# Optimization experiments

Measured on AMD Instinct MI355X. Metric: run time of the kernel, lower is better.

Reference implementation:

```python
import jax, jax.numpy as jnp
import numpy as np

B, L, D = 2, 2048, 2048
HQ, HKV = 32, 8
HD = D // HQ  # 64
ROPE_BASE = 10000.0
ROPE_SCALE = 1.0


def setup_inputs() -> dict:
    key = jax.random.key(0)
    ks = jax.random.split(key, 5)
    s = 0.02
    return {
        "x": jax.random.normal(ks[0], (B, L, D), dtype=jnp.float32),
        "pos_ids": jnp.arange(L, dtype=jnp.int64) if jax.config.jax_enable_x64 else jnp.arange(L, dtype=jnp.int32),
        "wq": jax.random.normal(ks[1], (D, D), dtype=jnp.float32) * s,
        "wk": jax.random.normal(ks[2], (HKV * HD, D), dtype=jnp.float32) * s,
        "wv": jax.random.normal(ks[3], (HKV * HD, D), dtype=jnp.float32) * s,
        "wo": jax.random.normal(ks[4], (D, D), dtype=jnp.float32) * s,
    }


def _rope_cos_sin(pos_ids, rot_dim, dtype):
    half = rot_dim // 2
    idx = jnp.arange(half, dtype=jnp.float32)
    inv_freq = (1.0 / (ROPE_BASE ** (idx / half))) * ROPE_SCALE  # [half]
    freqs = pos_ids.astype(dtype)[:, None] * inv_freq.astype(dtype)[None, :]  # [L, half]
    return jnp.cos(freqs), jnp.sin(freqs)


def _apply_rotary(x, cos, sin):
    # x: [B, L, H, Hd]; interleaved pair rotation on full head dim
    b, l, h, hd = x.shape
    xp = x.reshape(b, l, h, hd // 2, 2)
    x1, x2 = xp[..., 0], xp[..., 1]
    c = cos.reshape(1, l, 1, hd // 2)
    s = sin.reshape(1, l, 1, hd // 2)
    y1 = x1 * c - x2 * s
    y2 = x1 * s + x2 * c
    return jnp.stack([y1, y2], axis=-1).reshape(b, l, h, hd)


def reference(x, pos_ids, wq, wk, wv, wo):
    b, l, d = x.shape
    q = (x @ wq.T).reshape(b, l, HQ, HD)
    k = (x @ wk.T).reshape(b, l, HKV, HD)
    v = (x @ wv.T).reshape(b, l, HKV, HD)

    cos, sin = _rope_cos_sin(pos_ids, HD, x.dtype)
    q = _apply_rotary(q, cos, sin)
    k = _apply_rotary(k, cos, sin)

    group = HQ // HKV  # GQA: each kv head serves `group` consecutive q heads
    k = jnp.repeat(k, group, axis=2)  # [b, l, HQ, HD]
    v = jnp.repeat(v, group, axis=2)

    scale = 1.0 / jnp.sqrt(jnp.asarray(HD, dtype=x.dtype))
    scores = jnp.einsum("bqhd,bkhd->bhqk", q, k) * scale  # [b, HQ, l, l]
    causal = jnp.tril(jnp.ones((l, l), dtype=bool))
    neg = jnp.asarray(jnp.finfo(x.dtype).min, dtype=x.dtype)
    scores = jnp.where(causal[None, None], scores, neg)
    attn = jax.nn.softmax(scores, axis=-1)
    out = jnp.einsum("bhqk,bkhd->bqhd", attn, v).reshape(b, l, d)
    return out @ wo.T
```

## Files before the change

### kernel.cpp

```cpp
#include <hip/hip_runtime.h>
#include <stdint.h>

typedef unsigned short u16;
typedef unsigned int   u32;
typedef __bf16 bf16_t;
typedef bf16_t bf16x8 __attribute__((ext_vector_type(8)));
typedef u16    u16x8  __attribute__((ext_vector_type(8)));
typedef float  f32x4  __attribute__((ext_vector_type(4)));
typedef float  f32x16 __attribute__((ext_vector_type(16)));

#define NB   2
#define NL   2048
#define ND   2048
#define NHQ  32
#define NHKV 8
#define NHD  64
#define NQKV 3072
#define QSCALE 0.18033688011112042f
#define SM_SHIFT 24.0f

__device__ __forceinline__ u16 f2bf(float x){
  union{float f;u32 u;} v; v.f = x;
  u32 r = v.u + 0x7FFFu + ((v.u >> 16) & 1u);
  return (u16)(r >> 16);
}
__device__ __forceinline__ float bf2f(u16 b){
  union{u32 u;float f;} v; v.u = ((u32)b) << 16; return v.f;
}

__device__ __forceinline__ float exp2_hw(float x){
#if __has_builtin(__builtin_amdgcn_exp2f)
  return __builtin_amdgcn_exp2f(x);
#else
  float r; asm("v_exp_f32 %0, %1" : "=v"(r) : "v"(x)); return r;
#endif
}

__device__ __forceinline__ void gload_lds16(const void* g, void* l){
  auto gp = reinterpret_cast<__attribute__((address_space(1))) u16*>(
      (uintptr_t)g);
  auto lp = reinterpret_cast<__attribute__((address_space(3))) u16*>(
      (uintptr_t)l);
  __builtin_amdgcn_global_load_lds(gp, lp, 16, 0, 0);
}

__device__ __forceinline__ f32x4 mfma16(bf16x8 a, bf16x8 b, f32x4 c){
  return __builtin_amdgcn_mfma_f32_16x16x32_bf16(a, b, c, 0, 0, 0);
}
__device__ __forceinline__ f32x16 mfma32(bf16x8 a, bf16x8 b, f32x16 c){
  return __builtin_amdgcn_mfma_f32_32x32x16_bf16(a, b, c, 0, 0, 0);
}
__device__ __forceinline__ u32 cvtpk(float lo, float hi){
  u32 w;
  asm("v_cvt_pk_bf16_f32 %0, %1, %2" : "=v"(w) : "v"(lo), "v"(hi));
  return w;
}

template<int N> __device__ __forceinline__ void lgkm_wait(){
  if      constexpr (N == 0)  asm volatile("s_waitcnt lgkmcnt(0)"  ::: "memory");
  else if constexpr (N == 4)  asm volatile("s_waitcnt lgkmcnt(4)"  ::: "memory");
  else if constexpr (N == 8)  asm volatile("s_waitcnt lgkmcnt(8)"  ::: "memory");
  else if constexpr (N == 12) asm volatile("s_waitcnt lgkmcnt(12)" ::: "memory");
  else if constexpr (N == 14) asm volatile("s_waitcnt lgkmcnt(14)" ::: "memory");
  else                        asm volatile("s_waitcnt lgkmcnt(15)" ::: "memory");
  __builtin_amdgcn_sched_barrier(0);
}

#define CV_S1 2097152
#define CV_S2 3145728
#define CV_S3 3407872
#define CV_S4 3670016
#define CV_S5 4718592
#define CV_TOT (CV_S5 + 65536)

__global__ void k_prep(const float* __restrict__ x,  const float* __restrict__ wq,
                       const float* __restrict__ wk, const float* __restrict__ wv,
                       const float* __restrict__ wo, const int* __restrict__ pos,
                       u16* __restrict__ xb, u16* __restrict__ wqkvb, u16* __restrict__ wob,
                       float2* __restrict__ csT){
  int i = blockIdx.x * 256 + threadIdx.x;
  if (i < CV_S5){
    const float4* src; ushort4* dst; int off;
    if (i < CV_S1)      { src = (const float4*)x;  dst = (ushort4*)xb;    off = i; }
    else if (i < CV_S2) { src = (const float4*)wq; dst = (ushort4*)wqkvb; off = i - CV_S1; }
    else if (i < CV_S3) { src = (const float4*)wk; dst = (ushort4*)wqkvb + 1048576; off = i - CV_S2; }
    else if (i < CV_S4) { src = (const float4*)wv; dst = (ushort4*)wqkvb + 1310720; off = i - CV_S3; }
    else                { src = (const float4*)wo; dst = (ushort4*)wob;   off = i - CV_S4; }
    float4 f = src[off];
    ushort4 o;
    o.x = f2bf(f.x); o.y = f2bf(f.y); o.z = f2bf(f.z); o.w = f2bf(f.w);
    dst[off] = o;
  } else {
    int idx = i - CV_S5;
    int l = idx >> 5, k = idx & 31;
    float p = (float)pos[l];
    float inv = __expf(-((float)k * (1.0f/32.0f)) * 9.210340371976184f);
    float fr = p * inv;
    csT[idx] = make_float2(cosf(fr), sinf(fr));
  }
}

template<int BM, int BN, int MODE>
__global__ __launch_bounds__(512) void k_gemm9(const u16* __restrict__ A,
                                               const u16* __restrict__ Bm,
                                               void* __restrict__ Cp,
                                               u16* __restrict__ Qo, u16* __restrict__ Ko,
                                               u16* __restrict__ VT,
                                               const float2* __restrict__ csT,
                                               int M, int N, int K){
  constexpr int LA_N = BM/64;
  constexpr int LB_N = BN/64;
  constexpr int LN   = LA_N + LB_N;
  constexpr int MR   = BM/32;
  constexpr int MH   = MR/2;
  constexpr int NF   = BN/64;
  __shared__ u16 LAb[2][BM*64];
  __shared__ u16 LBb[2][BN*64];
  const int tid = threadIdx.x;
  const int lane = tid & 63, w = tid >> 6;
  const int wr = w >> 2, wc = w & 3;
  const int lr = lane & 15, lg = lane >> 4;
  const int tn = blockIdx.x * BN, tm = blockIdx.y * BM;
  const size_t Kb = (size_t)K * 2;
  const char* Ab = (const char*)A;
  const char* Bb = (const char*)Bm;

  u32 soff[LN]; int ldoff[LN];
#pragma unroll
  for (int l = 0; l < LN; ++l){
    int o = ((l < LA_N) ? l : (l - LA_N))*8192 + tid*16;
    int s = o ^ (((o>>7)&7)<<4);
    int row = s >> 7, col = s & 127;
    int trow = (l < LA_N) ? (tm + row) : (tn + row);
    soff[l]  = (u32)((size_t)trow * Kb + col);
    ldoff[l] = o;
  }
  const int c0 = ( lg      ^ (lr & 7)) << 4;
  const int c1 = ((4 + lg) ^ (lr & 7)) << 4;
  const int arow = (wr*(BM/2) + lr) * 128;
  const int brow = (wc*(BN/4) + lr) * 128;

  f32x4 acc[MR][NF] = {};
  bf16x8 bfA[NF][2], bfB[NF][2], afA[MH][2], afB[MH][2];
  const int NT = K >> 6;

#pragma unroll
  for (int l = 0; l < LN; ++l){
    char* base = (l < LA_N) ? (char*)LAb[0] : (char*)LBb[0];
    const char* gb = (l < LA_N) ? Ab : Bb;
    gload_lds16(gb + soff[l], base + ldoff[l]);
  }
  asm volatile("s_waitcnt vmcnt(0)" ::: "memory");
  __builtin_amdgcn_s_barrier();
#pragma unroll
  for (int n = 0; n < NF; ++n){
    bfA[n][0] = *(const bf16x8*)((const char*)LBb[0] + brow + n*2048 + c0);
    bfA[n][1] = *(const bf16x8*)((const char*)LBb[0] + brow + n*2048 + c1);
  }
#pragma unroll
  for (int q = 0; q < MH; ++q){
    afA[q][0] = *(const bf16x8*)((const char*)LAb[0] + arow + q*2048 + c0);
    afA[q][1] = *(const bf16x8*)((const char*)LAb[0] + arow + q*2048 + c1);
  }

#define TILE(laC, laN, lbN, bfc, bfn, PRE, KOFF)                            \
    {                                                                       \
      if (PRE){                                                             \
        _Pragma("unroll")                                                   \
        for (int l = 0; l < LN; ++l){                                       \
          char* nb_ = (l < LA_N) ? (char*)(laN) : (char*)(lbN);             \
          const char* gb_ = (l < LA_N) ? Ab : Bb;                           \
          gload_lds16(gb_ + soff[l] + (KOFF), nb_ + ldoff[l]);              \
        }                                                                   \
      }                                                                     \
      _Pragma("unroll")                                                     \
      for (int q = 0; q < MH; ++q){                                         \
        afB[q][0] = *(const bf16x8*)((const char*)(laC) + arow + (MH+q)*2048 + c0); \
        afB[q][1] = *(const bf16x8*)((const char*)(laC) + arow + (MH+q)*2048 + c1); \
      }                                                                     \
      lgkm_wait<2*MH>();                                                    \
      __builtin_amdgcn_s_setprio(1);                                        \
      _Pragma("unroll")                                                     \
      for (int q = 0; q < MH; ++q){                                         \
        _Pragma("unroll")                                                   \
        for (int n = 0; n < NF; ++n){                                       \
          acc[q][n] = mfma16(afA[q][0], bfc[n][0], acc[q][n]);              \
          acc[q][n] = mfma16(afA[q][1], bfc[n][1], acc[q][n]);              \
        }                                                                   \
      }                                                                     \
      __builtin_amdgcn_s_setprio(0);                                        \
      asm volatile("s_waitcnt vmcnt(0)" ::: "memory");                      \
      __builtin_amdgcn_s_barrier();                                         \
      if (PRE){                                                             \
        _Pragma("unroll")                                                   \
        for (int n = 0; n < NF; ++n){                                       \
          bfn[n][0] = *(const bf16x8*)((const char*)(lbN) + brow + n*2048 + c0); \
          bfn[n][1] = *(const bf16x8*)((const char*)(lbN) + brow + n*2048 + c1); \
        }                                                                   \
        _Pragma("unroll")                                                   \
        for (int q = 0; q < MH; ++q){                                       \
          afA[q][0] = *(const bf16x8*)((const char*)(laN) + arow + q*2048 + c0); \
          afA[q][1] = *(const bf16x8*)((const char*)(laN) + arow + q*2048 + c1); \
        }                                                                   \
        lgkm_wait<2*NF + 2*MH>();                                           \
      } else {                                                              \
        lgkm_wait<0>();                                                     \
      }                                                                     \
      __builtin_amdgcn_s_setprio(1);                                        \
      _Pragma("unroll")                                                     \
      for (int q = 0; q < MH; ++q){                                         \
        _Pragma("unroll")                                                   \
        for (int n = 0; n < NF; ++n){                                       \
          acc[MH+q][n] = mfma16(afB[q][0], bfc[n][0], acc[MH+q][n]);        \
          acc[MH+q][n] = mfma16(afB[q][1], bfc[n][1], acc[MH+q][n]);        \
        }                                                                   \
      }                                                                     \
      __builtin_amdgcn_s_setprio(0);                                        \
      __builtin_amdgcn_s_barrier();                                         \
    }

#pragma unroll 1
  for (int kt = 0; kt < NT; kt += 2){
    const bool pre1 = (kt + 2 < NT);
    TILE(LAb[0], LAb[1], LBb[1], bfA, bfB, true, (u32)(kt+1)*128)
    TILE(LAb[1], LAb[0], LBb[0], bfB, bfA, pre1, (u32)(kt+2)*128)
  }
#undef TILE

  const int rb = tm + wr*(BM/2) + lg*4;
  const int cb = tn + wc*(BN/4) + lr;
#pragma unroll
  for (int m = 0; m < MR; ++m){
#pragma unroll
    for (int n = 0; n < NF; ++n){
      const int col = cb + n*16;
      if (MODE == 2){
        const int row0 = rb + m*16;
        const int bb = row0 >> 11;
        if (col >= 2560){
          const int vcol = col - 2560, kvh = vcol >> 6, d = vcol & 63;
          const int l0 = row0 & 2047;
          ushort4 sv;
          sv.x = f2bf(acc[m][n][0]); sv.y = f2bf(acc[m][n][1]);
          sv.z = f2bf(acc[m][n][2]); sv.w = f2bf(acc[m][n][3]);
          *reinterpret_cast<ushort4*>(&VT[((size_t)(bb*NHKV + kvh)*NHD + d)*NL + l0]) = sv;
        } else {
          const bool isQ = col < 2048;
          const int hcol = isQ ? col : (col - 2048);
          const int hh = hcol >> 6, d = hcol & 63;
          const int i = (d >> 1);
          const bool odd = (d & 1);
          u16* dst = isQ ? &Qo[((size_t)(bb*NHQ + hh)*NL) * NHD]
                         : &Ko[((size_t)(bb*NHKV + hh)*NL) * NHD];
#pragma unroll
          for (int r = 0; r < 4; ++r){
            const int l = (row0 + r) & 2047;
            const float2 cs = csT[l*32 + i];
            const float a = acc[m][n][r];
            const float p = __shfl_xor(a, 1);
            float y = odd ? (p*cs.y + a*cs.x) : (a*cs.x - p*cs.y);
            if (isQ) y *= QSCALE;
            dst[(size_t)l*NHD + d] = f2bf(y);
          }
        }
      } else {
#pragma unroll
        for (int r = 0; r < 4; ++r){
          size_t off = (size_t)(rb + m*16 + r) * N + col;
          ((float*)Cp)[off] = acc[m][n][r];
        }
      }
    }
  }
}

__device__ __forceinline__ void stage_kv32(const u16* __restrict__ Kp, const u16* __restrict__ VTp,
                                           int kvb, u16* lk, u16* lv, int w, int lane){
  const char* ks = (const char*)(Kp + (size_t)kvb*NHD);
  const char* vs = (const char*)VTp + (size_t)kvb*2;
  const int o = w*1024 + lane*16;
  const int swk = o ^ (((o>>7)&7)<<4);
  gload_lds16(ks + swk, (char*)lk + w*1024);
  const int row = o >> 6, c = o & 63;
  gload_lds16(vs + (size_t)row*(NL*2) + (c ^ (((row>>1)&3)<<4)), (char*)lv + w*1024);
}
__device__ __forceinline__ bf16x8 ldsK(const u16* base, int row, int colb){
  return *reinterpret_cast<const bf16x8*>((const char*)base + row*128 + (colb ^ ((row&7)<<4)));
}
__device__ __forceinline__ bf16x8 ldsV(const u16* base, int row, int colb){
  return *reinterpret_cast<const bf16x8*>((const char*)base + row*64 + (colb ^ (((row>>1)&3)<<4)));
}

__global__ __launch_bounds__(256) void k_attn7(const u16* __restrict__ Q, const u16* __restrict__ Kg,
                                               const u16* __restrict__ VT, u16* __restrict__ O){
  __shared__ u16 LK[2][2048];
  __shared__ u16 LV[2][2048];
  const int tid = threadIdx.x, lane = tid & 63, w = tid >> 6;
  const int q32 = lane & 31, hi = lane >> 5;
  const int f = blockIdx.x;
  const int round = f >> 8, c = f & 255;
  const int i16 = c >> 4;
  const int qti = round*16 + ((round & 1) ? (15 - i16) : i16);
  const int qt = 63 - qti;
  const int grp = c & 15;
  const int b = grp >> 3, kvh = grp & 7;
  const int h = kvh*4 + w;
  const u16* Qp  = Q  + ((size_t)(b*NHQ  + h  ))*NL*NHD;
  const u16* Kp  = Kg + ((size_t)(b*NHKV + kvh))*NL*NHD;
  const u16* VTp = VT + ((size_t)(b*NHKV + kvh))*NHD*NL;

  const int qrow = qt*32 + q32;
  const int ntw  = qt + 1;

  bf16x8 qf[4];
#pragma unroll
  for (int ks = 0; ks < 4; ++ks)
    qf[ks] = *reinterpret_cast<const bf16x8*>(&Qp[(size_t)qrow*NHD + ks*16 + hi*8]);

  f32x16 o0 = {}, o1 = {};
  float lsum = 0.0f;

  stage_kv32(Kp, VTp, 0, LK[0], LV[0], w, lane);
  __syncthreads();

#pragma unroll 1
  for (int j = 0; j < ntw; ++j){
    const int cur = j & 1;
    const u16* lk = LK[cur];
    const u16* lv = LV[cur];
    if (j + 1 < ntw)
      stage_kv32(Kp, VTp, (j+1) << 5, LK[cur^1], LV[cur^1], w, lane);

    const int kvb = j << 5;
    bf16x8 kf[4];
#pragma unroll
    for (int ks = 0; ks < 4; ++ks)
      kf[ks] = ldsK(lk, q32, ks*32 + hi*16);
    f32x16 s0 = {};
    __builtin_amdgcn_s_setprio(1);
#pragma unroll
    for (int ks = 0; ks < 4; ++ks)
      s0 = mfma32(kf[ks], qf[ks], s0);
    __builtin_amdgcn_s_setprio(0);
    if (j == ntw - 1){
#pragma unroll
      for (int r = 0; r < 16; ++r){
        const int kl = (r&3) + 8*(r>>2) + 4*hi;
        if (kvb + kl > qrow) s0[r] = -1e30f;
      }
    }
#pragma unroll
    for (int r = 0; r < 16; ++r) s0[r] = exp2_hw(s0[r] - SM_SHIFT);
    float u[8];
#pragma unroll
    for (int r = 0; r < 8; ++r)  u[r] = s0[r] + s0[r+8];
#pragma unroll
    for (int r = 0; r < 4; ++r)  u[r] += u[r+4];
    lsum += (u[0]+u[1]) + (u[2]+u[3]);
    u32 wds[8];
#pragma unroll
    for (int i = 0; i < 8; ++i) wds[i] = cvtpk(s0[2*i], s0[2*i+1]);
    bf16x8 pf[2];
#pragma unroll
    for (int fi = 0; fi < 2; ++fi){
      u32 x  = wds[4*fi+0], y  = wds[4*fi+2];
      u32 x2 = wds[4*fi+1], y2 = wds[4*fi+3];
      asm("v_permlane32_swap_b32 %0, %1" : "+v"(x),  "+v"(y));
      asm("v_permlane32_swap_b32 %0, %1" : "+v"(x2), "+v"(y2));
      union { u32 wq[4]; bf16x8 v; } uu;
      uu.wq[0] = x; uu.wq[1] = x2; uu.wq[2] = y; uu.wq[3] = y2;
      pf[fi] = uu.v;
    }
    bf16x8 vf[4];
    vf[0] = ldsV(lv, q32,      hi*16);
    vf[1] = ldsV(lv, q32,      32 + hi*16);
    vf[2] = ldsV(lv, 32 + q32, hi*16);
    vf[3] = ldsV(lv, 32 + q32, 32 + hi*16);
    __builtin_amdgcn_s_setprio(1);
    o0 = mfma32(vf[0], pf[0], o0);
    o0 = mfma32(vf[1], pf[1], o0);
    o1 = mfma32(vf[2], pf[0], o1);
    o1 = mfma32(vf[3], pf[1], o1);
    __builtin_amdgcn_s_setprio(0);
    __syncthreads();
  }

  float lt = lsum + __shfl_xor(lsum, 32);
  const float inv = 1.0f / lt;
  u16* Op = O + ((size_t)(b*NL + qrow))*ND + h*NHD;
#pragma unroll
  for (int md = 0; md < 2; ++md){
#pragma unroll
    for (int q4 = 0; q4 < 4; ++q4){
      ushort4 sv;
      float a0 = (md ? o1[4*q4+0] : o0[4*q4+0]) * inv;
      float a1 = (md ? o1[4*q4+1] : o0[4*q4+1]) * inv;
      float a2 = (md ? o1[4*q4+2] : o0[4*q4+2]) * inv;
      float a3 = (md ? o1[4*q4+3] : o0[4*q4+3]) * inv;
      sv.x = f2bf(a0); sv.y = f2bf(a1); sv.z = f2bf(a2); sv.w = f2bf(a3);
      *reinterpret_cast<ushort4*>(&Op[md*32 + 8*q4 + 4*hi]) = sv;
    }
  }
}

extern "C" void kernel_launch(void* const* d_in, const int* in_sizes, int n_in,
                              void* d_out, int out_size, void* d_ws, size_t ws_size,
                              hipStream_t stream){
  (void)in_sizes; (void)n_in; (void)out_size; (void)ws_size;
  const float* x   = (const float*)d_in[0];
  const int*   pos = (const int*)  d_in[1];
  const float* wq  = (const float*)d_in[2];
  const float* wk  = (const float*)d_in[3];
  const float* wv  = (const float*)d_in[4];
  const float* wo  = (const float*)d_in[5];

  char* ws = (char*)d_ws;
  size_t off = 0;
  auto alloc = [&](size_t bytes) -> void* {
    void* p = ws + off;
    off += (bytes + 255) & ~(size_t)255;
    return p;
  };
  const size_t n_x   = (size_t)NB*NL*ND;
  const size_t n_wq  = (size_t)ND*ND;

  u16* xb    = (u16*)alloc(n_x*2);
  u16* wqkvb = (u16*)alloc((size_t)NQKV*ND*2);
  u16* wob   = (u16*)alloc(n_wq*2);
  u16* Qb    = (u16*)alloc((size_t)NB*NHQ*NL*NHD*2);
  u16* Kb    = (u16*)alloc((size_t)NB*NHKV*NL*NHD*2);
  u16* VTb   = (u16*)alloc((size_t)NB*NHKV*NHD*NL*2);
  float2* csT= (float2*)alloc((size_t)NL*32*8);

  k_prep<<<CV_TOT/256, 256, 0, stream>>>(x, wq, wk, wv, wo, pos, xb, wqkvb, wob, csT);

  k_gemm9<256,192,2><<<dim3(NQKV/192, (NB*NL)/256), 512, 0, stream>>>(
      xb, wqkvb, nullptr, Qb, Kb, VTb, csT, NB*NL, NQKV, ND);
  k_attn7<<<1024, 256, 0, stream>>>(Qb, Kb, VTb, xb);
  k_gemm9<256,128,0><<<dim3(ND/128, (NB*NL)/256), 512, 0, stream>>>(
      xb, wob, d_out, nullptr, nullptr, nullptr, nullptr, NB*NL, ND, ND);
}
```

Baseline: 172.0 us.

## Split attention KV loop across two wave groups and merge via LDS

The attention kernel now launches 512 threads per block. Two groups of four waves each process half of the causal KV tiles for the same query tile, using separate double-buffered LDS regions. The partial outputs and row sums are reduced through shared memory before the final normalisation and store. This shortens the serial KV loop per wave and raises the number of waves available for latency hiding. In exchange it adds the reduction step, more LDS use and per-iteration barriers over twice as many threads, with some idle waves when the tile count is odd.

```diff
diff --git a/kernel.cpp b/kernel.cpp
--- a/kernel.cpp
+++ b/kernel.cpp
@@ -275,14 +275,14 @@
 }
 
 __device__ __forceinline__ void stage_kv32(const u16* __restrict__ Kp, const u16* __restrict__ VTp,
-                                           int kvb, u16* lk, u16* lv, int w, int lane){
+                                           int kvb, u16* lk, u16* lv, int w4, int lane){
   const char* ks = (const char*)(Kp + (size_t)kvb*NHD);
   const char* vs = (const char*)VTp + (size_t)kvb*2;
-  const int o = w*1024 + lane*16;
+  const int o = w4*1024 + lane*16;
   const int swk = o ^ (((o>>7)&7)<<4);
-  gload_lds16(ks + swk, (char*)lk + w*1024);
+  gload_lds16(ks + swk, (char*)lk + w4*1024);
   const int row = o >> 6, c = o & 63;
-  gload_lds16(vs + (size_t)row*(NL*2) + (c ^ (((row>>1)&3)<<4)), (char*)lv + w*1024);
+  gload_lds16(vs + (size_t)row*(NL*2) + (c ^ (((row>>1)&3)<<4)), (char*)lv + w4*1024);
 }
 __device__ __forceinline__ bf16x8 ldsK(const u16* base, int row, int colb){
   return *reinterpret_cast<const bf16x8*>((const char*)base + row*128 + (colb ^ ((row&7)<<4)));
@@ -291,11 +291,11 @@
   return *reinterpret_cast<const bf16x8*>((const char*)base + row*64 + (colb ^ (((row>>1)&3)<<4)));
 }
 
-__global__ __launch_bounds__(256) void k_attn7(const u16* __restrict__ Q, const u16* __restrict__ Kg,
+__global__ __launch_bounds__(512) void k_attn8(const u16* __restrict__ Q, const u16* __restrict__ Kg,
                                                const u16* __restrict__ VT, u16* __restrict__ O){
-  __shared__ u16 LK[2][2048];
-  __shared__ u16 LV[2][2048];
+  __shared__ u16 SM[4][2][2048];
   const int tid = threadIdx.x, lane = tid & 63, w = tid >> 6;
+  const int hh = w & 3, stream = w >> 2;
   const int q32 = lane & 31, hi = lane >> 5;
   const int f = blockIdx.x;
   const int round = f >> 8, c = f & 255;
@@ -304,13 +304,20 @@
   const int qt = 63 - qti;
   const int grp = c & 15;
   const int b = grp >> 3, kvh = grp & 7;
-  const int h = kvh*4 + w;
+  const int h = kvh*4 + hh;
   const u16* Qp  = Q  + ((size_t)(b*NHQ  + h  ))*NL*NHD;
   const u16* Kp  = Kg + ((size_t)(b*NHKV + kvh))*NL*NHD;
   const u16* VTp = VT + ((size_t)(b*NHKV + kvh))*NHD*NL;
 
   const int qrow = qt*32 + q32;
   const int ntw  = qt + 1;
+  const int hL   = (ntw + 1) >> 1;
+  const int hU   = ntw - hL;
+  const int myN  = stream ? hU : hL;
+  const int base = stream ? hL : 0;
+
+  u16 (*LK)[2048] = stream ? SM[2] : SM[0];
+  u16 (*LV)[2048] = stream ? SM[3] : SM[1];
 
   bf16x8 qf[4];
 #pragma unroll
@@ -320,85 +327,112 @@
   f32x16 o0 = {}, o1 = {};
   float lsum = 0.0f;
 
-  stage_kv32(Kp, VTp, 0, LK[0], LV[0], w, lane);
+  if (myN > 0)
+    stage_kv32(Kp, VTp, base << 5, LK[0], LV[0], hh, lane);
   __syncthreads();
 
 #pragma unroll 1
-  for (int j = 0; j < ntw; ++j){
-    const int cur = j & 1;
+  for (int i = 0; i < hL; ++i){
+    const int cur = i & 1;
     const u16* lk = LK[cur];
     const u16* lv = LV[cur];
-    if (j + 1 < ntw)
-      stage_kv32(Kp, VTp, (j+1) << 5, LK[cur^1], LV[cur^1], w, lane);
-
-    const int kvb = j << 5;
-    bf16x8 kf[4];
-#pragma unroll
-    for (int ks = 0; ks < 4; ++ks)
-      kf[ks] = ldsK(lk, q32, ks*32 + hi*16);
-    f32x16 s0 = {};
-    __builtin_amdgcn_s_setprio(1);
-#pragma unroll
-    for (int ks = 0; ks < 4; ++ks)
-      s0 = mfma32(kf[ks], qf[ks], s0);
-    __builtin_amdgcn_s_setprio(0);
-    if (j == ntw - 1){
-#pragma unroll
-      for (int r = 0; r < 16; ++r){
-        const int kl = (r&3) + 8*(r>>2) + 4*hi;
-        if (kvb + kl > qrow) s0[r] = -1e30f;
+    if (i + 1 < myN)
+      stage_kv32(Kp, VTp, (base + i + 1) << 5, LK[cur^1], LV[cur^1], hh, lane);
+
+    if (i < myN){
+      const int jj  = base + i;
+      const int kvb = jj << 5;
+      bf16x8 kf[4];
+#pragma unroll
+      for (int ks = 0; ks < 4; ++ks)
+        kf[ks] = ldsK(lk, q32, ks*32 + hi*16);
+      f32x16 s0 = {};
+      __builtin_amdgcn_s_setprio(1);
+#pragma unroll
+      for (int ks = 0; ks < 4; ++ks)
+        s0 = mfma32(kf[ks], qf[ks], s0);
+      __builtin_amdgcn_s_setprio(0);
+      if (jj == ntw - 1){
+#pragma unroll
+        for (int r = 0; r < 16; ++r){
+          const int kl = (r&3) + 8*(r>>2) + 4*hi;
+          if (kvb + kl > qrow) s0[r] = -1e30f;
+        }
       }
+#pragma unroll
+      for (int r = 0; r < 16; ++r) s0[r] = exp2_hw(s0[r] - SM_SHIFT);
+      float u[8];
+#pragma unroll
+      for (int r = 0; r < 8; ++r)  u[r] = s0[r] + s0[r+8];
+#pragma unroll
+      for (int r = 0; r < 4; ++r)  u[r] += u[r+4];
+      lsum += (u[0]+u[1]) + (u[2]+u[3]);
+      u32 wds[8];
+#pragma unroll
+      for (int i2 = 0; i2 < 8; ++i2) wds[i2] = cvtpk(s0[2*i2], s0[2*i2+1]);
+      bf16x8 pf[2];
+#pragma unroll
+      for (int fi = 0; fi < 2; ++fi){
+        u32 x  = wds[4*fi+0], y  = wds[4*fi+2];
+        u32 x2 = wds[4*fi+1], y2 = wds[4*fi+3];
+        asm("v_permlane32_swap_b32 %0, %1" : "+v"(x),  "+v"(y));
+        asm("v_permlane32_swap_b32 %0, %1" : "+v"(x2), "+v"(y2));
+        union { u32 wq[4]; bf16x8 v; } uu;
+        uu.wq[0] = x; uu.wq[1] = x2; uu.wq[2] = y; uu.wq[3] = y2;
+        pf[fi] = uu.v;
+      }
+      bf16x8 vf[4];
+      vf[0] = ldsV(lv, q32,      hi*16);
+      vf[1] = ldsV(lv, q32,      32 + hi*16);
+      vf[2] = ldsV(lv, 32 + q32, hi*16);
+      vf[3] = ldsV(lv, 32 + q32, 32 + hi*16);
+      __builtin_amdgcn_s_setprio(1);
+      o0 = mfma32(vf[0], pf[0], o0);
+      o0 = mfma32(vf[1], pf[1], o0);
+      o1 = mfma32(vf[2], pf[0], o1);
+      o1 = mfma32(vf[3], pf[1], o1);
+      __builtin_amdgcn_s_setprio(0);
     }
-#pragma unroll
-    for (int r = 0; r < 16; ++r) s0[r] = exp2_hw(s0[r] - SM_SHIFT);
-    float u[8];
-#pragma unroll
-    for (int r = 0; r < 8; ++r)  u[r] = s0[r] + s0[r+8];
-#pragma unroll
-    for (int r = 0; r < 4; ++r)  u[r] += u[r+4];
-    lsum += (u[0]+u[1]) + (u[2]+u[3]);
-    u32 wds[8];
-#pragma unroll
-    for (int i = 0; i < 8; ++i) wds[i] = cvtpk(s0[2*i], s0[2*i+1]);
-    bf16x8 pf[2];
-#pragma unroll
-    for (int fi = 0; fi < 2; ++fi){
-      u32 x  = wds[4*fi+0], y  = wds[4*fi+2];
-      u32 x2 = wds[4*fi+1], y2 = wds[4*fi+3];
-      asm("v_permlane32_swap_b32 %0, %1" : "+v"(x),  "+v"(y));
-      asm("v_permlane32_swap_b32 %0, %1" : "+v"(x2), "+v"(y2));
-      union { u32 wq[4]; bf16x8 v; } uu;
-      uu.wq[0] = x; uu.wq[1] = x2; uu.wq[2] = y; uu.wq[3] = y2;
-      pf[fi] = uu.v;
-    }
-    bf16x8 vf[4];
-    vf[0] = ldsV(lv, q32,      hi*16);
-    vf[1] = ldsV(lv, q32,      32 + hi*16);
-    vf[2] = ldsV(lv, 32 + q32, hi*16);
-    vf[3] = ldsV(lv, 32 + q32, 32 + hi*16);
-    __builtin_amdgcn_s_setprio(1);
-    o0 = mfma32(vf[0], pf[0], o0);
-    o0 = mfma32(vf[1], pf[1], o0);
-    o1 = mfma32(vf[2], pf[0], o1);
-    o1 = mfma32(vf[3], pf[1], o1);
-    __builtin_amdgcn_s_setprio(0);
     __syncthreads();
   }
 
-  float lt = lsum + __shfl_xor(lsum, 32);
-  const float inv = 1.0f / lt;
-  u16* Op = O + ((size_t)(b*NL + qrow))*ND + h*NHD;
-#pragma unroll
-  for (int md = 0; md < 2; ++md){
-#pragma unroll
-    for (int q4 = 0; q4 < 4; ++q4){
-      ushort4 sv;
-      float a0 = (md ? o1[4*q4+0] : o0[4*q4+0]) * inv;
-      float a1 = (md ? o1[4*q4+1] : o0[4*q4+1]) * inv;
-      float a2 = (md ? o1[4*q4+2] : o0[4*q4+2]) * inv;
-      float a3 = (md ? o1[4*q4+3] : o0[4*q4+3]) * inv;
-      sv.x = f2bf(a0); sv.y = f2bf(a1); sv.z = f2bf(a2); sv.w = f2bf(a3);
-      *reinterpret_cast<ushort4*>(&Op[md*32 + 8*q4 + 4*hi]) = sv;
+  float* S = (float*)SM;
+  if (stream == 1){
+#pragma unroll
+    for (int r = 0; r < 16; ++r) S[r*256 + hh*64 + lane] = o0[r];
+    S[4096 + hh*64 + lane] = lsum;
+  }
+  __syncthreads();
+  if (stream == 0){
+#pragma unroll
+    for (int r = 0; r < 16; ++r) o0[r] += S[r*256 + hh*64 + lane];
+    lsum += S[4096 + hh*64 + lane];
+  }
+  __syncthreads();
+  if (stream == 1){
+#pragma unroll
+    for (int r = 0; r < 16; ++r) S[r*256 + hh*64 + lane] = o1[r];
+  }
+  __syncthreads();
+  if (stream == 0){
+#pragma unroll
+    for (int r = 0; r < 16; ++r) o1[r] += S[r*256 + hh*64 + lane];
+
+    float lt = lsum + __shfl_xor(lsum, 32);
+    const float inv = 1.0f / lt;
+    u16* Op = O + ((size_t)(b*NL + qrow))*ND + h*NHD;
+#pragma unroll
+    for (int md = 0; md < 2; ++md){
+#pragma unroll
+      for (int q4 = 0; q4 < 4; ++q4){
+        ushort4 sv;
+        float a0 = (md ? o1[4*q4+0] : o0[4*q4+0]) * inv;
+        float a1 = (md ? o1[4*q4+1] : o0[4*q4+1]) * inv;
+        float a2 = (md ? o1[4*q4+2] : o0[4*q4+2]) * inv;
+        float a3 = (md ? o1[4*q4+3] : o0[4*q4+3]) * inv;
+        sv.x = f2bf(a0); sv.y = f2bf(a1); sv.z = f2bf(a2); sv.w = f2bf(a3);
+        *reinterpret_cast<ushort4*>(&Op[md*32 + 8*q4 + 4*hi]) = sv;
+      }
     }
   }
 }
@@ -436,7 +470,7 @@
 
   k_gemm9<256,192,2><<<dim3(NQKV/192, (NB*NL)/256), 512, 0, stream>>>(
       xb, wqkvb, nullptr, Qb, Kb, VTb, csT, NB*NL, NQKV, ND);
-  k_attn7<<<1024, 256, 0, stream>>>(Qb, Kb, VTb, xb);
+  k_attn8<<<1024, 512, 0, stream>>>(Qb, Kb, VTb, xb);
   k_gemm9<256,128,0><<<dim3(ND/128, (NB*NL)/256), 512, 0, stream>>>(
       xb, wob, d_out, nullptr, nullptr, nullptr, nullptr, NB*NL, ND, ND);
 }
```

New measurement: 172.8 us. No clear change (+0.5%).

## Triple-buffer GEMM LDS tiles with two-ahead prefetch and shrink QKV tile

Applied to the files above, without the earlier changes.

Moves the GEMM main loop from double to triple buffering in LDS. Global-to-LDS loads are issued two k-tiles ahead, and only the older batch is waited on (vmcnt(LN)), so load latency can overlap more compute. The QKV projection tile width drops from 192 to 128, which keeps LDS use within budget and raises the block count. The cost is more LDS per block, which may lower occupancy, and smaller tiles give less reuse per load.

```diff
diff --git a/kernel.cpp b/kernel.cpp
--- a/kernel.cpp
+++ b/kernel.cpp
@@ -63,6 +63,12 @@
   else if constexpr (N == 12) asm volatile("s_waitcnt lgkmcnt(12)" ::: "memory");
   else if constexpr (N == 14) asm volatile("s_waitcnt lgkmcnt(14)" ::: "memory");
   else                        asm volatile("s_waitcnt lgkmcnt(15)" ::: "memory");
+  __builtin_amdgcn_sched_barrier(0);
+}
+template<int N> __device__ __forceinline__ void vm_wait(){
+  if      constexpr (N == 0)  asm volatile("s_waitcnt vmcnt(0)" ::: "memory");
+  else if constexpr (N == 6)  asm volatile("s_waitcnt vmcnt(6)" ::: "memory");
+  else                        asm volatile("s_waitcnt vmcnt(8)" ::: "memory");
   __builtin_amdgcn_sched_barrier(0);
 }
 
@@ -114,8 +120,10 @@
   constexpr int MR   = BM/32;
   constexpr int MH   = MR/2;
   constexpr int NF   = BN/64;
-  __shared__ u16 LAb[2][BM*64];
-  __shared__ u16 LBb[2][BN*64];
+  constexpr int ASZ  = BM*64;
+  constexpr int BSZ  = BN*64;
+  __shared__ u16 LAb[3][ASZ];
+  __shared__ u16 LBb[3][BSZ];
   const int tid = threadIdx.x;
   const int lane = tid & 63, w = tid >> 6;
   const int wr = w >> 2, wc = w & 3;
@@ -150,7 +158,13 @@
     const char* gb = (l < LA_N) ? Ab : Bb;
     gload_lds16(gb + soff[l], base + ldoff[l]);
   }
-  asm volatile("s_waitcnt vmcnt(0)" ::: "memory");
+#pragma unroll
+  for (int l = 0; l < LN; ++l){
+    char* base = (l < LA_N) ? (char*)LAb[1] : (char*)LBb[1];
+    const char* gb = (l < LA_N) ? Ab : Bb;
+    gload_lds16(gb + soff[l] + 128, base + ldoff[l]);
+  }
+  vm_wait<LN>();
   __builtin_amdgcn_s_barrier();
 #pragma unroll
   for (int n = 0; n < NF; ++n){
@@ -163,67 +177,80 @@
     afA[q][1] = *(const bf16x8*)((const char*)LAb[0] + arow + q*2048 + c1);
   }
 
-#define TILE(laC, laN, lbN, bfc, bfn, PRE, KOFF)                            \
-    {                                                                       \
-      if (PRE){                                                             \
-        _Pragma("unroll")                                                   \
-        for (int l = 0; l < LN; ++l){                                       \
-          char* nb_ = (l < LA_N) ? (char*)(laN) : (char*)(lbN);             \
-          const char* gb_ = (l < LA_N) ? Ab : Bb;                           \
-          gload_lds16(gb_ + soff[l] + (KOFF), nb_ + ldoff[l]);              \
-        }                                                                   \
-      }                                                                     \
-      _Pragma("unroll")                                                     \
-      for (int q = 0; q < MH; ++q){                                         \
-        afB[q][0] = *(const bf16x8*)((const char*)(laC) + arow + (MH+q)*2048 + c0); \
-        afB[q][1] = *(const bf16x8*)((const char*)(laC) + arow + (MH+q)*2048 + c1); \
-      }                                                                     \
-      lgkm_wait<2*MH>();                                                    \
-      __builtin_amdgcn_s_setprio(1);                                        \
-      _Pragma("unroll")                                                     \
-      for (int q = 0; q < MH; ++q){                                         \
-        _Pragma("unroll")                                                   \
-        for (int n = 0; n < NF; ++n){                                       \
-          acc[q][n] = mfma16(afA[q][0], bfc[n][0], acc[q][n]);              \
-          acc[q][n] = mfma16(afA[q][1], bfc[n][1], acc[q][n]);              \
-        }                                                                   \
-      }                                                                     \
-      __builtin_amdgcn_s_setprio(0);                                        \
-      asm volatile("s_waitcnt vmcnt(0)" ::: "memory");                      \
-      __builtin_amdgcn_s_barrier();                                         \
-      if (PRE){                                                             \
-        _Pragma("unroll")                                                   \
-        for (int n = 0; n < NF; ++n){                                       \
-          bfn[n][0] = *(const bf16x8*)((const char*)(lbN) + brow + n*2048 + c0); \
-          bfn[n][1] = *(const bf16x8*)((const char*)(lbN) + brow + n*2048 + c1); \
-        }                                                                   \
-        _Pragma("unroll")                                                   \
-        for (int q = 0; q < MH; ++q){                                       \
-          afA[q][0] = *(const bf16x8*)((const char*)(laN) + arow + q*2048 + c0); \
-          afA[q][1] = *(const bf16x8*)((const char*)(laN) + arow + q*2048 + c1); \
-        }                                                                   \
-        lgkm_wait<2*NF + 2*MH>();                                           \
-      } else {                                                              \
-        lgkm_wait<0>();                                                     \
-      }                                                                     \
-      __builtin_amdgcn_s_setprio(1);                                        \
-      _Pragma("unroll")                                                     \
-      for (int q = 0; q < MH; ++q){                                         \
-        _Pragma("unroll")                                                   \
-        for (int n = 0; n < NF; ++n){                                       \
-          acc[MH+q][n] = mfma16(afB[q][0], bfc[n][0], acc[MH+q][n]);        \
-          acc[MH+q][n] = mfma16(afB[q][1], bfc[n][1], acc[MH+q][n]);        \
-        }                                                                   \
-      }                                                                     \
-      __builtin_amdgcn_s_setprio(0);                                        \
-      __builtin_amdgcn_s_barrier();                                         \
+  int iC = 0, iN = 1, iI = 2;
+
+#define TILE(bfc, bfn, KT)                                                    \
+    {                                                                         \
+      const bool issue = ((KT) + 2 < NT);                                     \
+      const bool readn = ((KT) + 1 < NT);                                     \
+      const char* la = (const char*)LAb[iC] + arow;                           \
+      const char* lb = (const char*)LBb[iC] + brow;                           \
+          \
+      if (issue){                                                             \
+        char* aI = (char*)LAb[iI];                                            \
+        char* bI = (char*)LBb[iI];                                            \
+        const u32 koff = (u32)((KT)+2) * 128;                                 \
+        _Pragma("unroll")                                                     \
+        for (int l = 0; l < LN; ++l){                                         \
+          char* nb_ = (l < LA_N) ? aI : bI;                                   \
+          const char* gb_ = (l < LA_N) ? Ab : Bb;                             \
+          gload_lds16(gb_ + soff[l] + koff, nb_ + ldoff[l]);                  \
+        }                                                                     \
+      }                                                                       \
+      _Pragma("unroll")                                                       \
+      for (int q = 0; q < MH; ++q){                                           \
+        afB[q][0] = *(const bf16x8*)(la + (MH+q)*2048 + c0);                  \
+        afB[q][1] = *(const bf16x8*)(la + (MH+q)*2048 + c1);                  \
+      }                                                                       \
+      lgkm_wait<2*MH>();                                                      \
+      __builtin_amdgcn_s_setprio(1);                                          \
+      _Pragma("unroll")                                                       \
+      for (int q = 0; q < MH; ++q){                                           \
+        _Pragma("unroll")                                                     \
+        for (int n = 0; n < NF; ++n){                                         \
+          acc[q][n] = mfma16(afA[q][0], bfc[n][0], acc[q][n]);                \
+          acc[q][n] = mfma16(afA[q][1], bfc[n][1], acc[q][n]);                \
+        }                                                                     \
+      }                                                                       \
+      __builtin_amdgcn_s_setprio(0);                                          \
+      if (issue) vm_wait<LN>(); else vm_wait<0>();    \
+      __builtin_amdgcn_s_barrier();                                           \
+                \
+      if (readn){                                                             \
+        const char* laN_ = (const char*)LAb[iN] + arow;                       \
+        const char* lbN_ = (const char*)LBb[iN] + brow;                       \
+        _Pragma("unroll")                                                     \
+        for (int n = 0; n < NF; ++n){                                         \
+          bfn[n][0] = *(const bf16x8*)(lbN_ + n*2048 + c0);                   \
+          bfn[n][1] = *(const bf16x8*)(lbN_ + n*2048 + c1);                   \
+        }                                                                     \
+        _Pragma("unroll")                                                     \
+        for (int q = 0; q < MH; ++q){                                         \
+          afA[q][0] = *(const bf16x8*)(laN_ + q*2048 + c0);                   \
+          afA[q][1] = *(const bf16x8*)(laN_ + q*2048 + c1);                   \
+        }                                                                     \
+        lgkm_wait<2*NF + 2*MH>();                                             \
+      } else {                                                                \
+        lgkm_wait<0>();                                                       \
+      }                                                                       \
+      __builtin_amdgcn_s_setprio(1);                                          \
+      _Pragma("unroll")                                                       \
+      for (int q = 0; q < MH; ++q){                                           \
+        _Pragma("unroll")                                                     \
+        for (int n = 0; n < NF; ++n){                                         \
+          acc[MH+q][n] = mfma16(afB[q][0], bfc[n][0], acc[MH+q][n]);          \
+          acc[MH+q][n] = mfma16(afB[q][1], bfc[n][1], acc[MH+q][n]);          \
+        }                                                                     \
+      }                                                                       \
+      __builtin_amdgcn_s_setprio(0);                                          \
+      __builtin_amdgcn_s_barrier();                                           \
+      { int t_ = iC; iC = iN; iN = iI; iI = t_; }         \
     }
 
 #pragma unroll 1
   for (int kt = 0; kt < NT; kt += 2){
-    const bool pre1 = (kt + 2 < NT);
-    TILE(LAb[0], LAb[1], LBb[1], bfA, bfB, true, (u32)(kt+1)*128)
-    TILE(LAb[1], LAb[0], LBb[0], bfB, bfA, pre1, (u32)(kt+2)*128)
+    TILE(bfA, bfB, kt)
+    TILE(bfB, bfA, kt+1)
   }
 #undef TILE
 
@@ -434,7 +461,7 @@
 
   k_prep<<<CV_TOT/256, 256, 0, stream>>>(x, wq, wk, wv, wo, pos, xb, wqkvb, wob, csT);
 
-  k_gemm9<256,192,2><<<dim3(NQKV/192, (NB*NL)/256), 512, 0, stream>>>(
+  k_gemm9<256,128,2><<<dim3(NQKV/128, (NB*NL)/256), 512, 0, stream>>>(
       xb, wqkvb, nullptr, Qb, Kb, VTb, csT, NB*NL, NQKV, ND);
   k_attn7<<<1024, 256, 0, stream>>>(Qb, Kb, VTb, xb);
   k_gemm9<256,128,0><<<dim3(ND/128, (NB*NL)/256), 512, 0, stream>>>(
```

New measurement: 186.3 us. 8.4% more time.
